# Kernel tuning notes

Hardware: AMD Instinct MI355X
Metric: run time of the kernel (lower is better)

## Reference

```python
import jax, jax.numpy as jnp
import numpy as np

EMBED = 1024
HEADS = 16
HEAD_DIM = EMBED // HEADS  # 64


def setup_inputs() -> dict:
    key = jax.random.key(0)
    ks = jax.random.split(key, 10)
    B, SQ, SK = 2, 2048, 2048
    s = 0.02
    return {
        "decoder_hidden_state": jax.random.normal(ks[0], (B, SQ, EMBED), jnp.float32),
        "encoder_hidden_state": jax.random.normal(ks[1], (B, SK, EMBED), jnp.float32),
        # per-head Q/K/V projections, stacked over heads [H, E, Dh]
        "wq": jax.random.normal(ks[2], (HEADS, EMBED, HEAD_DIM), jnp.float32) * s,
        "bq": jax.random.normal(ks[3], (HEADS, HEAD_DIM), jnp.float32) * s,
        "wk": jax.random.normal(ks[4], (HEADS, EMBED, HEAD_DIM), jnp.float32) * s,
        "bk": jax.random.normal(ks[5], (HEADS, HEAD_DIM), jnp.float32) * s,
        "wv": jax.random.normal(ks[6], (HEADS, EMBED, HEAD_DIM), jnp.float32) * s,
        "bv": jax.random.normal(ks[7], (HEADS, HEAD_DIM), jnp.float32) * s,
        # output projection [E, E] and bias [E]
        "wo": jax.random.normal(ks[8], (EMBED, EMBED), jnp.float32) * s,
        "bo": jax.random.normal(ks[9], (EMBED,), jnp.float32) * s,
    }


def reference(decoder_hidden_state, encoder_hidden_state, wq, bq, wk, bk, wv, bv, wo, bo):
    # Q from decoder, K/V from encoder (cross-attention), batched over heads.
    q = jnp.einsum("bqe,hed->bhqd", decoder_hidden_state, wq) + bq[None, :, None, :]
    k = jnp.einsum("bke,hed->bhkd", encoder_hidden_state, wk) + bk[None, :, None, :]
    v = jnp.einsum("bke,hed->bhkd", encoder_hidden_state, wv) + bv[None, :, None, :]
    scale = 1.0 / jnp.sqrt(jnp.asarray(HEAD_DIM, q.dtype))
    scores = jnp.einsum("bhqd,bhkd->bhqk", q, k) * scale  # [B,H,Sq,Sk]
    attn = jax.nn.softmax(scores, axis=-1)
    ctx = jnp.einsum("bhqk,bhkd->bhqd", attn, v)
    B, H, SQ, D = ctx.shape
    # concat heads along last dim (head-major order, matching torch.cat)
    ctx = jnp.transpose(ctx, (0, 2, 1, 3)).reshape(B, SQ, H * D)
    return ctx @ wo + bo
```

## Files before the change

kernel.cpp:

```cpp
#include <hip/hip_runtime.h>
#include <cstdint>


typedef unsigned short u16;
typedef unsigned int   u32;
typedef __bf16 bf16x8 __attribute__((ext_vector_type(8)));
typedef float  f32x4  __attribute__((ext_vector_type(4)));
typedef float  f32x16 __attribute__((ext_vector_type(16)));

#define SEQ 2048
#define EMB 1024
#define NROWS 4096
#define QSCL 0.18033688011112042f

__device__ __forceinline__ u16 f2b(float f) {
    u32 u = __builtin_bit_cast(u32, f);
    return (u16)((u + 0x7FFFu + ((u >> 16) & 1u)) >> 16);
}

__device__ __forceinline__ u32 cvtpk(float a, float b) {
    u32 r; asm("v_cvt_pk_bf16_f32 %0, %1, %2" : "=v"(r) : "v"(a), "v"(b)); return r;
}

__device__ __forceinline__ float exp2g(float x) {
    float r; asm("v_exp_f32 %0, %1" : "=v"(r) : "v"(x)); return r;
}

__device__ __forceinline__ int swz_off(int lin) {
    int row = lin >> 6;
    return lin ^ ((((row) + (row >> 2)) & 3) << 4);
}

#define GLDS16(src, dst) __builtin_amdgcn_global_load_lds( \
    (const __attribute__((address_space(1))) void*)(src),  \
    (__attribute__((address_space(3))) void*)(dst), 16, 0, 0)

__global__ __launch_bounds__(256) void convx_kernel(const float* __restrict__ in,
                                                    u16* __restrict__ out, int n4) {
    int i = blockIdx.x * 256 + threadIdx.x;
    if (i < n4) {
        float4 v = ((const float4*)in)[i];
        uint2 o;
        o.x = (u32)f2b(v.x) | ((u32)f2b(v.y) << 16);
        o.y = (u32)f2b(v.z) | ((u32)f2b(v.w) << 16);
        ((uint2*)out)[i] = o;
    }
}

__global__ __launch_bounds__(256) void convw_kernel(const float* __restrict__ in,
                                                    u16* __restrict__ out, int mode) {
    __shared__ u16 T[64][72];
    int tile = blockIdx.x;
    int r  = threadIdx.x >> 2;
    int c0 = (threadIdx.x & 3) * 16;
    int h = 0, e0, n0 = 0;
    size_t srcBase; int srcStride;
    if (mode == 0) { h = tile >> 4; e0 = (tile & 15) * 64; srcBase = ((size_t)h * 1024 + e0) * 64; srcStride = 64; }
    else           { n0 = (tile >> 4) * 64; e0 = (tile & 15) * 64; srcBase = (size_t)e0 * 1024 + n0; srcStride = 1024; }
    const float* src = in + srcBase + (size_t)r * srcStride + c0;
    #pragma unroll
    for (int i = 0; i < 16; i += 4) {
        float4 v = *(const float4*)(src + i);
        T[c0 + i][r]     = f2b(v.x);
        T[c0 + i + 1][r] = f2b(v.y);
        T[c0 + i + 2][r] = f2b(v.z);
        T[c0 + i + 3][r] = f2b(v.w);
    }
    __syncthreads();
    int rr = threadIdx.x >> 2, cc = (threadIdx.x & 3) * 16;
    size_t dstBase = (mode == 0) ? ((size_t)(h * 64 + rr) * 1024 + e0)
                                 : ((size_t)(n0 + rr) * 1024 + e0);
    uint4* dst = (uint4*)(out + dstBase + cc);
    const u16* srow = &T[rr][cc];
    dst[0] = *(const uint4*)(srow);
    dst[1] = *(const uint4*)(srow + 8);
}

__global__ __launch_bounds__(256, 2) void gemm_qkv(const u16* __restrict__ XdecB,
                                                   const u16* __restrict__ XencB,
                                                   const u16* __restrict__ WqT,
                                                   const u16* __restrict__ WkT,
                                                   const u16* __restrict__ WvT,
                                                   const float* __restrict__ bq,
                                                   const float* __restrict__ bk,
                                                   const float* __restrict__ bv,
                                                   u16* __restrict__ Qbuf,
                                                   u16* __restrict__ Kbuf,
                                                   u16* __restrict__ Vtb) {
    __shared__ __align__(16) u16 SH[17408];
    int bid0 = blockIdx.x;
    int bid  = (bid0 & 7) * 96 + (bid0 >> 3);

    const u16 *Ap, *Btp; const float* bias; u16* outp;
    int m0, n0, mode; float scale;
    if (bid < 256) {
        Ap = XdecB; Btp = WqT; bias = bq; outp = Qbuf; mode = 1; scale = QSCL;
        m0 = (bid >> 3) * 128; n0 = (bid & 7) * 128;
    } else {
        int kv = bid - 256; m0 = (kv >> 4) * 128; int nt = kv & 15; Ap = XencB; scale = 1.0f;
        if (nt < 8) { Btp = WkT; bias = bk; outp = Kbuf; mode = 1; n0 = nt * 128; }
        else        { Btp = WvT; bias = bv; outp = Vtb; mode = 2; n0 = (nt - 8) * 128; }
    }

    const int t = threadIdx.x, lane = t & 63, w = t >> 6;
    const int wr = (w >> 1) * 64, wc = (w & 1) * 64;
    const int fr = lane & 15, k0 = (lane >> 4) * 8, rr = (lane >> 4) * 4;

    const u16* srcA[2]; const u16* srcB[2]; int dstL[2];
    #pragma unroll
    for (int c = 0; c < 2; ++c) {
        int lin = c * 4096 + t * 16;
        int lo  = swz_off(lin);
        srcA[c] = Ap  + (size_t)(m0 + (lo >> 6)) * 1024 + ((lo & 63) >> 1);
        srcB[c] = Btp + (size_t)(n0 + (lo >> 6)) * 1024 + ((lo & 63) >> 1);
        dstL[c] = lin;
    }
    int aoff[4], boff[4];
    #pragma unroll
    for (int m = 0; m < 4; ++m) aoff[m] = swz_off((wr + m * 16 + fr) * 64 + k0 * 2);
    #pragma unroll
    for (int n = 0; n < 4; ++n) boff[n] = swz_off((wc + n * 16 + fr) * 64 + k0 * 2);

    f32x4 acc[4][4] = {};

    #define ASB(b) ((char*)SH + (b) * 8192)
    #define BSB(b) ((char*)SH + 16384 + (b) * 8192)

    #pragma unroll
    for (int c = 0; c < 2; ++c) {
        GLDS16(srcA[c], ASB(0) + dstL[c]);
        GLDS16(srcB[c], BSB(0) + dstL[c]);
    }
    __syncthreads();

    for (int kt = 0; kt < 32; ++kt) {
        const char* Ab = ASB(kt & 1);
        const char* Bb = BSB(kt & 1);
        bf16x8 af[4], bfr[4];
        #pragma unroll
        for (int m = 0; m < 4; ++m) af[m]  = *(const bf16x8*)(Ab + aoff[m]);
        #pragma unroll
        for (int n = 0; n < 4; ++n) bfr[n] = *(const bf16x8*)(Bb + boff[n]);
        if (kt + 1 < 32) {
            char* An = ASB((kt + 1) & 1);
            char* Bn = BSB((kt + 1) & 1);
            int ko = (kt + 1) * 32;
            #pragma unroll
            for (int c = 0; c < 2; ++c) {
                GLDS16(srcA[c] + ko, An + dstL[c]);
                GLDS16(srcB[c] + ko, Bn + dstL[c]);
            }
        }
        #pragma unroll
        for (int m = 0; m < 4; ++m)
            #pragma unroll
            for (int n = 0; n < 4; ++n)
                acc[m][n] = __builtin_amdgcn_mfma_f32_16x16x32_bf16(af[m], bfr[n], acc[m][n], 0, 0, 0);
        __syncthreads();
    }

    if (mode == 1 || mode == 0) {
        #pragma unroll
        for (int m = 0; m < 4; ++m) {
            int row = m0 + wr + m * 16 + rr;
            #pragma unroll
            for (int n = 0; n < 4; ++n) {
                int col = n0 + wc + n * 16 + fr;
                float bv = bias[col];
                #pragma unroll
                for (int rg = 0; rg < 4; ++rg) {
                    float v = (acc[m][n][rg] + bv) * scale;
                    int rowg = row + rg;
                    int b = rowg >> 11, s = rowg & 2047;
                    int h = col >> 6, d = col & 63;
                    outp[(((size_t)b * 16 + h) * SEQ + s) * 64 + d] = f2b(v);
                }
            }
        }
    } else {
        u16* TR = SH;
        #pragma unroll
        for (int m = 0; m < 4; ++m) {
            int srow = wr + m * 16 + rr;
            #pragma unroll
            for (int n = 0; n < 4; ++n) {
                int dcol = wc + n * 16 + fr;
                float bv = bias[n0 + dcol];
                u32 lo = cvtpk(acc[m][n][0] + bv, acc[m][n][1] + bv);
                u32 hi = cvtpk(acc[m][n][2] + bv, acc[m][n][3] + bv);
                uint2 pr = {lo, hi};
                *(uint2*)(TR + dcol * 136 + srow) = pr;
            }
        }
        __syncthreads();
        int dcol = t >> 1, hf = t & 1;
        int col = n0 + dcol;
        int h = col >> 6, d = col & 63;
        int b = m0 >> 11, s0 = (m0 & 2047) + hf * 64;
        u16* dst = Vtb + (((size_t)b * 16 + h) * 64 + d) * SEQ + s0;
        const u16* srowp = TR + dcol * 136 + hf * 64;
        #pragma unroll
        for (int i = 0; i < 8; ++i)
            ((uint4*)dst)[i] = *(const uint4*)(srowp + i * 8);
    }
    #undef ASB
    #undef BSB
}

__global__ __launch_bounds__(256, 2) void gemm_out(const u16* __restrict__ A,
                                                   const u16* __restrict__ Bt,
                                                   const float* __restrict__ bias,
                                                   float* __restrict__ out) {
    __shared__ __align__(16) u16 As[2][128 * 32];
    __shared__ __align__(16) u16 Bs[2][64 * 32];
    int bid0 = blockIdx.x;
    int bid  = (bid0 & 7) * 64 + (bid0 >> 3);
    int m0 = (bid >> 4) * 128, n0 = (bid & 15) * 64;

    const int t = threadIdx.x, lane = t & 63, w = t >> 6;
    const int wr = w * 32;
    const int fr = lane & 15, k0 = (lane >> 4) * 8, rr = (lane >> 4) * 4;

    const u16* srcA[2]; int dstA[2];
    #pragma unroll
    for (int c = 0; c < 2; ++c) {
        int lin = c * 4096 + t * 16;
        int lo  = swz_off(lin);
        srcA[c] = A + (size_t)(m0 + (lo >> 6)) * 1024 + ((lo & 63) >> 1);
        dstA[c] = lin;
    }
    int linB = t * 16, loB = swz_off(linB);
    const u16* srcBp = Bt + (size_t)(n0 + (loB >> 6)) * 1024 + ((loB & 63) >> 1);

    int aoff[2], boff[4];
    #pragma unroll
    for (int m = 0; m < 2; ++m) aoff[m] = swz_off((wr + m * 16 + fr) * 64 + k0 * 2);
    #pragma unroll
    for (int n = 0; n < 4; ++n) boff[n] = swz_off((n * 16 + fr) * 64 + k0 * 2);

    f32x4 acc[2][4] = {};

    #pragma unroll
    for (int c = 0; c < 2; ++c) GLDS16(srcA[c], (char*)As[0] + dstA[c]);
    GLDS16(srcBp, (char*)Bs[0] + linB);
    __syncthreads();

    for (int kt = 0; kt < 32; ++kt) {
        const char* Ab = (const char*)As[kt & 1];
        const char* Bb = (const char*)Bs[kt & 1];
        bf16x8 af[2], bfr[4];
        #pragma unroll
        for (int m = 0; m < 2; ++m) af[m]  = *(const bf16x8*)(Ab + aoff[m]);
        #pragma unroll
        for (int n = 0; n < 4; ++n) bfr[n] = *(const bf16x8*)(Bb + boff[n]);
        if (kt + 1 < 32) {
            int ko = (kt + 1) * 32;
            char* An = (char*)As[(kt + 1) & 1];
            char* Bn = (char*)Bs[(kt + 1) & 1];
            #pragma unroll
            for (int c = 0; c < 2; ++c) GLDS16(srcA[c] + ko, An + dstA[c]);
            GLDS16(srcBp + ko, Bn + linB);
        }
        #pragma unroll
        for (int m = 0; m < 2; ++m)
            #pragma unroll
            for (int n = 0; n < 4; ++n)
                acc[m][n] = __builtin_amdgcn_mfma_f32_16x16x32_bf16(af[m], bfr[n], acc[m][n], 0, 0, 0);
        __syncthreads();
    }

    #pragma unroll
    for (int m = 0; m < 2; ++m) {
        int row = m0 + wr + m * 16 + rr;
        #pragma unroll
        for (int n = 0; n < 4; ++n) {
            int col = n0 + n * 16 + fr;
            float bv = bias[col];
            #pragma unroll
            for (int rg = 0; rg < 4; ++rg)
                out[(size_t)(row + rg) * EMB + col] = acc[m][n][rg] + bv;
        }
    }
}

__global__ __launch_bounds__(256, 2) void attn_kernel(const u16* __restrict__ Qb,
                                                      const u16* __restrict__ Kb,
                                                      const u16* __restrict__ Vt,
                                                      u16* __restrict__ Ctx) {
    __shared__ __align__(16) u16 KS[2][64 * 64];
    __shared__ __align__(16) u16 VS[2][64 * 64];
    int id0 = blockIdx.x;
    int id  = (id0 & 7) * 64 + (id0 >> 3);
    int qt = id & 15, bh = id >> 4;
    const int t = threadIdx.x, lane = t & 63, w = t >> 6;
    const int ql = lane & 31, hi = lane >> 5;
    const int q0 = qt * 128 + w * 32;

    const u16* Qp = Qb + (size_t)bh * SEQ * 64;
    const u16* Kp = Kb + (size_t)bh * SEQ * 64;
    const u16* Vp = Vt + (size_t)bh * 64 * SEQ;

    bf16x8 qf[4];
    #pragma unroll
    for (int s = 0; s < 4; ++s)
        qf[s] = *(const bf16x8*)(Qp + (size_t)(q0 + ql) * 64 + s * 16 + hi * 8);

    const u16* ksrc[2]; const u16* vsrc[2]; int linc[2];
    #pragma unroll
    for (int c = 0; c < 2; ++c) {
        int lin = c * 4096 + t * 16;
        int row = lin >> 7;
        int lo  = lin ^ ((row & 7) << 4);
        int colE = (lo & 127) >> 1;
        linc[c] = lin;
        ksrc[c] = Kp + (size_t)row * 64 + colE;
        vsrc[c] = Vp + (size_t)row * SEQ + colE;
    }

#define STAGE(buf, kb) do {                                            \
    _Pragma("unroll") for (int c = 0; c < 2; ++c)                      \
        GLDS16(ksrc[c] + (size_t)(kb) * 64, (char*)KS[buf] + linc[c]); \
    _Pragma("unroll") for (int c = 0; c < 2; ++c)                      \
        GLDS16(vsrc[c] + (kb),              (char*)VS[buf] + linc[c]); \
} while (0)

    int koff[2][4], voff[2][2][2];
    #pragma unroll
    for (int hh = 0; hh < 2; ++hh) {
        #pragma unroll
        for (int s = 0; s < 4; ++s)
            koff[hh][s] = ((hh * 32 + ql) * 128 + s * 32 + hi * 16) ^ ((ql & 7) << 4);
        #pragma unroll
        for (int n = 0; n < 2; ++n)
            #pragma unroll
            for (int s2 = 0; s2 < 2; ++s2)
                voff[hh][n][s2] = ((ql + n * 32) * 128 + hh * 64 + s2 * 32 + hi * 16) ^ ((ql & 7) << 4);
    }

    f32x16 acc0 = {}, acc1 = {};
    float lsum = 0.f;

#define COMPUTE(buf, hh) do {                                                    \
    bf16x8 kf0 = *(const bf16x8*)((const char*)KS[buf] + koff[hh][0]);           \
    bf16x8 kf1 = *(const bf16x8*)((const char*)KS[buf] + koff[hh][1]);           \
    bf16x8 kf2 = *(const bf16x8*)((const char*)KS[buf] + koff[hh][2]);           \
    bf16x8 kf3 = *(const bf16x8*)((const char*)KS[buf] + koff[hh][3]);           \
    f32x16 st0 = {}, st1 = {};                                                   \
    st0 = __builtin_amdgcn_mfma_f32_32x32x16_bf16(kf0, qf[0], st0, 0, 0, 0);     \
    st1 = __builtin_amdgcn_mfma_f32_32x32x16_bf16(kf1, qf[1], st1, 0, 0, 0);     \
    st0 = __builtin_amdgcn_mfma_f32_32x32x16_bf16(kf2, qf[2], st0, 0, 0, 0);     \
    st1 = __builtin_amdgcn_mfma_f32_32x32x16_bf16(kf3, qf[3], st1, 0, 0, 0);     \
    float p[16];                                                                 \
    _Pragma("unroll") for (int r = 0; r < 16; ++r) {                             \
        p[r] = exp2g(st0[r] + st1[r]); lsum += p[r];                             \
    }                                                                            \
    _Pragma("unroll") for (int s2 = 0; s2 < 2; ++s2) {                           \
        u32 a0 = cvtpk(p[8 * s2 + 0], p[8 * s2 + 1]);                            \
        u32 a1 = cvtpk(p[8 * s2 + 2], p[8 * s2 + 3]);                            \
        u32 a2 = cvtpk(p[8 * s2 + 4], p[8 * s2 + 5]);                            \
        u32 a3 = cvtpk(p[8 * s2 + 6], p[8 * s2 + 7]);                            \
        asm("v_permlane32_swap_b32 %0, %1" : "+v"(a0), "+v"(a2));                \
        asm("v_permlane32_swap_b32 %0, %1" : "+v"(a1), "+v"(a3));                \
        uint4 pkv = {a0, a1, a2, a3};                                            \
        bf16x8 pa = __builtin_bit_cast(bf16x8, pkv);                             \
        bf16x8 v0 = *(const bf16x8*)((const char*)VS[buf] + voff[hh][0][s2]);    \
        bf16x8 v1 = *(const bf16x8*)((const char*)VS[buf] + voff[hh][1][s2]);    \
        acc0 = __builtin_amdgcn_mfma_f32_32x32x16_bf16(pa, v0, acc0, 0, 0, 0);   \
        acc1 = __builtin_amdgcn_mfma_f32_32x32x16_bf16(pa, v1, acc1, 0, 0, 0);   \
    }                                                                            \
} while (0)

    STAGE(0, 0);
    __syncthreads();
    for (int it = 0; it < 32; ++it) {
        int cur = it & 1;
        if (it < 31) STAGE(cur ^ 1, (it + 1) * 64);
        COMPUTE(cur, 0);
        COMPUTE(cur, 1);
        __syncthreads();
    }

    lsum += __shfl_xor(lsum, 32, 64);
    float inv = 1.0f / lsum;
    size_t obase = (size_t)(bh >> 4) * SEQ * EMB + (bh & 15) * 64 + ql;
    #pragma unroll
    for (int r = 0; r < 16; ++r) {
        int qr = (r & 3) + 8 * (r >> 2) + 4 * hi;
        float iv = __shfl(inv, qr, 64);
        size_t off = obase + (size_t)(q0 + qr) * EMB;
        Ctx[off]      = f2b(acc0[r] * iv);
        Ctx[off + 32] = f2b(acc1[r] * iv);
    }
}

extern "C" void kernel_launch(void* const* d_in, const int* in_sizes, int n_in,
                              void* d_out, int out_size, void* d_ws, size_t ws_size,
                              hipStream_t stream) {
    const float* Xdec = (const float*)d_in[0];
    const float* Xenc = (const float*)d_in[1];
    const float* wq = (const float*)d_in[2];
    const float* bq = (const float*)d_in[3];
    const float* wk = (const float*)d_in[4];
    const float* bk = (const float*)d_in[5];
    const float* wv = (const float*)d_in[6];
    const float* bv = (const float*)d_in[7];
    const float* wo = (const float*)d_in[8];
    const float* bo = (const float*)d_in[9];

    char* ws = (char*)d_ws;
    const size_t MB = 1024ull * 1024ull;
    u16* XdecB = (u16*)(ws + 0 * MB);
    u16* XencB = (u16*)(ws + 8 * MB);
    u16* WqT   = (u16*)(ws + 16 * MB);
    u16* WkT   = (u16*)(ws + 18 * MB);
    u16* WvT   = (u16*)(ws + 20 * MB);
    u16* WoT   = (u16*)(ws + 22 * MB);
    u16* Qbuf  = (u16*)(ws + 24 * MB);
    u16* Kbuf  = (u16*)(ws + 32 * MB);
    u16* Vtb   = (u16*)(ws + 40 * MB);
    u16* CtxB  = (u16*)(ws + 48 * MB);

    convx_kernel<<<4096, 256, 0, stream>>>(Xdec, XdecB, NROWS * EMB / 4);
    convx_kernel<<<4096, 256, 0, stream>>>(Xenc, XencB, NROWS * EMB / 4);
    convw_kernel<<<256, 256, 0, stream>>>(wq, WqT, 0);
    convw_kernel<<<256, 256, 0, stream>>>(wk, WkT, 0);
    convw_kernel<<<256, 256, 0, stream>>>(wv, WvT, 0);
    convw_kernel<<<256, 256, 0, stream>>>(wo, WoT, 1);

    gemm_qkv<<<768, 256, 0, stream>>>(XdecB, XencB, WqT, WkT, WvT, bq, bk, bv,
                                      Qbuf, Kbuf, Vtb);

    attn_kernel<<<512, 256, 0, stream>>>(Qbuf, Kbuf, Vtb, CtxB);

    gemm_out<<<512, 256, 0, stream>>>(CtxB, WoT, bo, (float*)d_out);
}
```

Baseline: 212.4 us.

## Merge conversion launches, retime GEMM prefetch waits, double attention rows per warp

```diff
diff --git a/kernel.cpp b/kernel.cpp
--- a/kernel.cpp
+++ b/kernel.cpp
@@ -35,22 +35,38 @@
     (const __attribute__((address_space(1))) void*)(src),  \
     (__attribute__((address_space(3))) void*)(dst), 16, 0, 0)
 
-__global__ __launch_bounds__(256) void convx_kernel(const float* __restrict__ in,
-                                                    u16* __restrict__ out, int n4) {
+#define VMCNT(n) asm volatile("s_waitcnt vmcnt(" #n ")" ::: "memory")
+#define SBAR()   __builtin_amdgcn_s_barrier()
+#define SCHED0() __builtin_amdgcn_sched_barrier(0)
+
+__global__ __launch_bounds__(256) void convx2_kernel(const float* __restrict__ a,
+                                                     const float* __restrict__ b,
+                                                     u16* __restrict__ oa,
+                                                     u16* __restrict__ ob) {
     int i = blockIdx.x * 256 + threadIdx.x;
-    if (i < n4) {
-        float4 v = ((const float4*)in)[i];
-        uint2 o;
-        o.x = (u32)f2b(v.x) | ((u32)f2b(v.y) << 16);
-        o.y = (u32)f2b(v.z) | ((u32)f2b(v.w) << 16);
-        ((uint2*)out)[i] = o;
-    }
-}
-
-__global__ __launch_bounds__(256) void convw_kernel(const float* __restrict__ in,
-                                                    u16* __restrict__ out, int mode) {
+    const float* src; u16* dst; int j;
+    if (i < 1048576) { src = a; dst = oa; j = i; }
+    else             { src = b; dst = ob; j = i - 1048576; }
+    float4 v = ((const float4*)src)[j];
+    uint2 o;
+    o.x = (u32)f2b(v.x) | ((u32)f2b(v.y) << 16);
+    o.y = (u32)f2b(v.z) | ((u32)f2b(v.w) << 16);
+    ((uint2*)dst)[j] = o;
+}
+
+__global__ __launch_bounds__(256) void convw4_kernel(const float* __restrict__ wq,
+                                                     const float* __restrict__ wk,
+                                                     const float* __restrict__ wv,
+                                                     const float* __restrict__ wo,
+                                                     u16* __restrict__ oq,
+                                                     u16* __restrict__ ok,
+                                                     u16* __restrict__ ov,
+                                                     u16* __restrict__ oo) {
     __shared__ u16 T[64][72];
-    int tile = blockIdx.x;
+    int which = blockIdx.x >> 8, tile = blockIdx.x & 255;
+    const float* in = (which == 0) ? wq : (which == 1) ? wk : (which == 2) ? wv : wo;
+    u16* out = (which == 0) ? oq : (which == 1) ? ok : (which == 2) ? ov : oo;
+    int mode = (which == 3) ? 1 : 0;
     int r  = threadIdx.x >> 2;
     int c0 = (threadIdx.x & 3) * 16;
     int h = 0, e0, n0 = 0;
@@ -125,38 +141,33 @@
 
     #define ASB(b) ((char*)SH + (b) * 8192)
     #define BSB(b) ((char*)SH + 16384 + (b) * 8192)
-
-    #pragma unroll
-    for (int c = 0; c < 2; ++c) {
-        GLDS16(srcA[c], ASB(0) + dstL[c]);
-        GLDS16(srcB[c], BSB(0) + dstL[c]);
-    }
-    __syncthreads();
-
+    #define QSTAGE(buf, ko) do {                               \
+        _Pragma("unroll") for (int c = 0; c < 2; ++c) {        \
+            GLDS16(srcA[c] + (ko), ASB(buf) + dstL[c]);        \
+            GLDS16(srcB[c] + (ko), BSB(buf) + dstL[c]);        \
+        }                                                      \
+    } while (0)
+
+    QSTAGE(0, 0);
     for (int kt = 0; kt < 32; ++kt) {
-        const char* Ab = ASB(kt & 1);
-        const char* Bb = BSB(kt & 1);
+        int cur = kt & 1;
+        if (kt) SBAR();
+        if (kt + 1 < 32) { QSTAGE(cur ^ 1, (kt + 1) * 32); VMCNT(4); }
+        else             { VMCNT(0); }
+        SBAR();
+        SCHED0();
+        const char* Ab = ASB(cur);
+        const char* Bb = BSB(cur);
         bf16x8 af[4], bfr[4];
         #pragma unroll
         for (int m = 0; m < 4; ++m) af[m]  = *(const bf16x8*)(Ab + aoff[m]);
         #pragma unroll
         for (int n = 0; n < 4; ++n) bfr[n] = *(const bf16x8*)(Bb + boff[n]);
-        if (kt + 1 < 32) {
-            char* An = ASB((kt + 1) & 1);
-            char* Bn = BSB((kt + 1) & 1);
-            int ko = (kt + 1) * 32;
-            #pragma unroll
-            for (int c = 0; c < 2; ++c) {
-                GLDS16(srcA[c] + ko, An + dstL[c]);
-                GLDS16(srcB[c] + ko, Bn + dstL[c]);
-            }
-        }
         #pragma unroll
         for (int m = 0; m < 4; ++m)
             #pragma unroll
             for (int n = 0; n < 4; ++n)
                 acc[m][n] = __builtin_amdgcn_mfma_f32_16x16x32_bf16(af[m], bfr[n], acc[m][n], 0, 0, 0);
-        __syncthreads();
     }
 
     if (mode == 1 || mode == 0) {
@@ -178,6 +189,7 @@
             }
         }
     } else {
+        __syncthreads();
         u16* TR = SH;
         #pragma unroll
         for (int m = 0; m < 4; ++m) {
@@ -240,34 +252,34 @@
 
     f32x4 acc[2][4] = {};
 
-    #pragma unroll
-    for (int c = 0; c < 2; ++c) GLDS16(srcA[c], (char*)As[0] + dstA[c]);
-    GLDS16(srcBp, (char*)Bs[0] + linB);
-    __syncthreads();
-
+    #define OSTAGE(buf, ko) do {                                          \
+        _Pragma("unroll") for (int c = 0; c < 2; ++c)                     \
+            GLDS16(srcA[c] + (ko), (char*)As[buf] + dstA[c]);             \
+        GLDS16(srcBp + (ko), (char*)Bs[buf] + linB);                      \
+    } while (0)
+
+    OSTAGE(0, 0);
     for (int kt = 0; kt < 32; ++kt) {
-        const char* Ab = (const char*)As[kt & 1];
-        const char* Bb = (const char*)Bs[kt & 1];
+        int cur = kt & 1;
+        if (kt) SBAR();
+        if (kt + 1 < 32) { OSTAGE(cur ^ 1, (kt + 1) * 32); VMCNT(3); }
+        else             { VMCNT(0); }
+        SBAR();
+        SCHED0();
+        const char* Ab = (const char*)As[cur];
+        const char* Bb = (const char*)Bs[cur];
         bf16x8 af[2], bfr[4];
         #pragma unroll
         for (int m = 0; m < 2; ++m) af[m]  = *(const bf16x8*)(Ab + aoff[m]);
         #pragma unroll
         for (int n = 0; n < 4; ++n) bfr[n] = *(const bf16x8*)(Bb + boff[n]);
-        if (kt + 1 < 32) {
-            int ko = (kt + 1) * 32;
-            char* An = (char*)As[(kt + 1) & 1];
-            char* Bn = (char*)Bs[(kt + 1) & 1];
-            #pragma unroll
-            for (int c = 0; c < 2; ++c) GLDS16(srcA[c] + ko, An + dstA[c]);
-            GLDS16(srcBp + ko, Bn + linB);
-        }
         #pragma unroll
         for (int m = 0; m < 2; ++m)
             #pragma unroll
             for (int n = 0; n < 4; ++n)
                 acc[m][n] = __builtin_amdgcn_mfma_f32_16x16x32_bf16(af[m], bfr[n], acc[m][n], 0, 0, 0);
-        __syncthreads();
-    }
+    }
+    #undef OSTAGE
 
     #pragma unroll
     for (int m = 0; m < 2; ++m) {
@@ -283,27 +295,29 @@
     }
 }
 
-__global__ __launch_bounds__(256, 2) void attn_kernel(const u16* __restrict__ Qb,
+__global__ __launch_bounds__(256, 1) void attn_kernel(const u16* __restrict__ Qb,
                                                       const u16* __restrict__ Kb,
                                                       const u16* __restrict__ Vt,
                                                       u16* __restrict__ Ctx) {
     __shared__ __align__(16) u16 KS[2][64 * 64];
     __shared__ __align__(16) u16 VS[2][64 * 64];
     int id0 = blockIdx.x;
-    int id  = (id0 & 7) * 64 + (id0 >> 3);
-    int qt = id & 15, bh = id >> 4;
+    int id  = (id0 & 7) * 32 + (id0 >> 3);
+    int qt = id & 7, bh = id >> 3;
     const int t = threadIdx.x, lane = t & 63, w = t >> 6;
     const int ql = lane & 31, hi = lane >> 5;
-    const int q0 = qt * 128 + w * 32;
+    const int q0 = qt * 256 + w * 64;
 
     const u16* Qp = Qb + (size_t)bh * SEQ * 64;
     const u16* Kp = Kb + (size_t)bh * SEQ * 64;
     const u16* Vp = Vt + (size_t)bh * 64 * SEQ;
 
-    bf16x8 qf[4];
-    #pragma unroll
-    for (int s = 0; s < 4; ++s)
-        qf[s] = *(const bf16x8*)(Qp + (size_t)(q0 + ql) * 64 + s * 16 + hi * 8);
+    bf16x8 qfA[4], qfB[4];
+    #pragma unroll
+    for (int s = 0; s < 4; ++s) {
+        qfA[s] = *(const bf16x8*)(Qp + (size_t)(q0 + ql) * 64 + s * 16 + hi * 8);
+        qfB[s] = *(const bf16x8*)(Qp + (size_t)(q0 + 32 + ql) * 64 + s * 16 + hi * 8);
+    }
 
     const u16* ksrc[2]; const u16* vsrc[2]; int linc[2];
     #pragma unroll
@@ -337,59 +351,84 @@
                 voff[hh][n][s2] = ((ql + n * 32) * 128 + hh * 64 + s2 * 32 + hi * 16) ^ ((ql & 7) << 4);
     }
 
-    f32x16 acc0 = {}, acc1 = {};
-    float lsum = 0.f;
+    f32x16 aA0 = {}, aA1 = {}, aB0 = {}, aB1 = {};
+    float lsA = 0.f, lsB = 0.f;
+
+#define PACK8(PA, P, o) do {                                           \
+    u32 a0 = cvtpk(P[(o) + 0], P[(o) + 1]);                            \
+    u32 a1 = cvtpk(P[(o) + 2], P[(o) + 3]);                            \
+    u32 a2 = cvtpk(P[(o) + 4], P[(o) + 5]);                            \
+    u32 a3 = cvtpk(P[(o) + 6], P[(o) + 7]);                            \
+    asm("v_permlane32_swap_b32 %0, %1" : "+v"(a0), "+v"(a2));          \
+    asm("v_permlane32_swap_b32 %0, %1" : "+v"(a1), "+v"(a3));          \
+    uint4 pkv = {a0, a1, a2, a3};                                      \
+    PA = __builtin_bit_cast(bf16x8, pkv);                              \
+} while (0)
 
 #define COMPUTE(buf, hh) do {                                                    \
     bf16x8 kf0 = *(const bf16x8*)((const char*)KS[buf] + koff[hh][0]);           \
     bf16x8 kf1 = *(const bf16x8*)((const char*)KS[buf] + koff[hh][1]);           \
     bf16x8 kf2 = *(const bf16x8*)((const char*)KS[buf] + koff[hh][2]);           \
     bf16x8 kf3 = *(const bf16x8*)((const char*)KS[buf] + koff[hh][3]);           \
-    f32x16 st0 = {}, st1 = {};                                                   \
-    st0 = __builtin_amdgcn_mfma_f32_32x32x16_bf16(kf0, qf[0], st0, 0, 0, 0);     \
-    st1 = __builtin_amdgcn_mfma_f32_32x32x16_bf16(kf1, qf[1], st1, 0, 0, 0);     \
-    st0 = __builtin_amdgcn_mfma_f32_32x32x16_bf16(kf2, qf[2], st0, 0, 0, 0);     \
-    st1 = __builtin_amdgcn_mfma_f32_32x32x16_bf16(kf3, qf[3], st1, 0, 0, 0);     \
-    float p[16];                                                                 \
+    f32x16 s0 = {}, s1 = {};                                                     \
+    s0 = __builtin_amdgcn_mfma_f32_32x32x16_bf16(kf0, qfA[0], s0, 0, 0, 0);      \
+    s1 = __builtin_amdgcn_mfma_f32_32x32x16_bf16(kf1, qfA[1], s1, 0, 0, 0);      \
+    s0 = __builtin_amdgcn_mfma_f32_32x32x16_bf16(kf2, qfA[2], s0, 0, 0, 0);      \
+    s1 = __builtin_amdgcn_mfma_f32_32x32x16_bf16(kf3, qfA[3], s1, 0, 0, 0);      \
+    float pA[16];                                                                \
     _Pragma("unroll") for (int r = 0; r < 16; ++r) {                             \
-        p[r] = exp2g(st0[r] + st1[r]); lsum += p[r];                             \
+        pA[r] = exp2g(s0[r] + s1[r]); lsA += pA[r];                              \
+    }                                                                            \
+    f32x16 t0 = {}, t1 = {};                                                     \
+    t0 = __builtin_amdgcn_mfma_f32_32x32x16_bf16(kf0, qfB[0], t0, 0, 0, 0);      \
+    t1 = __builtin_amdgcn_mfma_f32_32x32x16_bf16(kf1, qfB[1], t1, 0, 0, 0);      \
+    t0 = __builtin_amdgcn_mfma_f32_32x32x16_bf16(kf2, qfB[2], t0, 0, 0, 0);      \
+    t1 = __builtin_amdgcn_mfma_f32_32x32x16_bf16(kf3, qfB[3], t1, 0, 0, 0);      \
+    float pB[16];                                                                \
+    _Pragma("unroll") for (int r = 0; r < 16; ++r) {                             \
+        pB[r] = exp2g(t0[r] + t1[r]); lsB += pB[r];                              \
     }                                                                            \
     _Pragma("unroll") for (int s2 = 0; s2 < 2; ++s2) {                           \
-        u32 a0 = cvtpk(p[8 * s2 + 0], p[8 * s2 + 1]);                            \
-        u32 a1 = cvtpk(p[8 * s2 + 2], p[8 * s2 + 3]);                            \
-        u32 a2 = cvtpk(p[8 * s2 + 4], p[8 * s2 + 5]);                            \
-        u32 a3 = cvtpk(p[8 * s2 + 6], p[8 * s2 + 7]);                            \
-        asm("v_permlane32_swap_b32 %0, %1" : "+v"(a0), "+v"(a2));                \
-        asm("v_permlane32_swap_b32 %0, %1" : "+v"(a1), "+v"(a3));                \
-        uint4 pkv = {a0, a1, a2, a3};                                            \
-        bf16x8 pa = __builtin_bit_cast(bf16x8, pkv);                             \
+        bf16x8 paA, paB;                                                         \
+        PACK8(paA, pA, 8 * s2);                                                  \
+        PACK8(paB, pB, 8 * s2);                                                  \
         bf16x8 v0 = *(const bf16x8*)((const char*)VS[buf] + voff[hh][0][s2]);    \
         bf16x8 v1 = *(const bf16x8*)((const char*)VS[buf] + voff[hh][1][s2]);    \
-        acc0 = __builtin_amdgcn_mfma_f32_32x32x16_bf16(pa, v0, acc0, 0, 0, 0);   \
-        acc1 = __builtin_amdgcn_mfma_f32_32x32x16_bf16(pa, v1, acc1, 0, 0, 0);   \
+        aA0 = __builtin_amdgcn_mfma_f32_32x32x16_bf16(paA, v0, aA0, 0, 0, 0);    \
+        aA1 = __builtin_amdgcn_mfma_f32_32x32x16_bf16(paA, v1, aA1, 0, 0, 0);    \
+        aB0 = __builtin_amdgcn_mfma_f32_32x32x16_bf16(paB, v0, aB0, 0, 0, 0);    \
+        aB1 = __builtin_amdgcn_mfma_f32_32x32x16_bf16(paB, v1, aB1, 0, 0, 0);    \
     }                                                                            \
 } while (0)
 
     STAGE(0, 0);
-    __syncthreads();
     for (int it = 0; it < 32; ++it) {
         int cur = it & 1;
-        if (it < 31) STAGE(cur ^ 1, (it + 1) * 64);
+        if (it) SBAR();
+        if (it < 31) { STAGE(cur ^ 1, (it + 1) * 64); VMCNT(4); }
+        else         { VMCNT(0); }
+        SBAR();
+        SCHED0();
         COMPUTE(cur, 0);
         COMPUTE(cur, 1);
-        __syncthreads();
-    }
-
-    lsum += __shfl_xor(lsum, 32, 64);
-    float inv = 1.0f / lsum;
-    size_t obase = (size_t)(bh >> 4) * SEQ * EMB + (bh & 15) * 64 + ql;
+    }
+
+    lsA += __shfl_xor(lsA, 32, 64);
+    lsB += __shfl_xor(lsB, 32, 64);
+    float invA = 1.0f / lsA, invB = 1.0f / lsB;
+    int b = bh >> 4, h = bh & 15;
+    size_t obase = (size_t)b * SEQ * EMB + h * 64 + ql;
     #pragma unroll
     for (int r = 0; r < 16; ++r) {
         int qr = (r & 3) + 8 * (r >> 2) + 4 * hi;
-        float iv = __shfl(inv, qr, 64);
-        size_t off = obase + (size_t)(q0 + qr) * EMB;
-        Ctx[off]      = f2b(acc0[r] * iv);
-        Ctx[off + 32] = f2b(acc1[r] * iv);
+        float ivA = __shfl(invA, qr, 64);
+        float ivB = __shfl(invB, qr, 64);
+        size_t offA = obase + (size_t)(q0 + qr) * EMB;
+        size_t offB = obase + (size_t)(q0 + 32 + qr) * EMB;
+        Ctx[offA]      = f2b(aA0[r] * ivA);
+        Ctx[offA + 32] = f2b(aA1[r] * ivA);
+        Ctx[offB]      = f2b(aB0[r] * ivB);
+        Ctx[offB + 32] = f2b(aB1[r] * ivB);
     }
 }
 
@@ -420,17 +459,13 @@
     u16* Vtb   = (u16*)(ws + 40 * MB);
     u16* CtxB  = (u16*)(ws + 48 * MB);
 
-    convx_kernel<<<4096, 256, 0, stream>>>(Xdec, XdecB, NROWS * EMB / 4);
-    convx_kernel<<<4096, 256, 0, stream>>>(Xenc, XencB, NROWS * EMB / 4);
-    convw_kernel<<<256, 256, 0, stream>>>(wq, WqT, 0);
-    convw_kernel<<<256, 256, 0, stream>>>(wk, WkT, 0);
-    convw_kernel<<<256, 256, 0, stream>>>(wv, WvT, 0);
-    convw_kernel<<<256, 256, 0, stream>>>(wo, WoT, 1);
+    convx2_kernel<<<8192, 256, 0, stream>>>(Xdec, Xenc, XdecB, XencB);
+    convw4_kernel<<<1024, 256, 0, stream>>>(wq, wk, wv, wo, WqT, WkT, WvT, WoT);
 
     gemm_qkv<<<768, 256, 0, stream>>>(XdecB, XencB, WqT, WkT, WvT, bq, bk, bv,
                                       Qbuf, Kbuf, Vtb);
 
-    attn_kernel<<<512, 256, 0, stream>>>(Qbuf, Kbuf, Vtb, CtxB);
+    attn_kernel<<<256, 256, 0, stream>>>(Qbuf, Kbuf, Vtb, CtxB);
 
     gemm_out<<<512, 256, 0, stream>>>(CtxB, WoT, bo, (float*)d_out);
 }
```

Result: slower. 220.5 us (+3.8%).
